# Kernel optimization log

Hardware: AMD Instinct MI355X
Metric: run time of the kernel (lower is better)

The kernel has to match this reference:

```python
import jax, jax.numpy as jnp
import numpy as np

B, T, D, H = 32, 512, 512, 1024


def setup_inputs() -> dict:
    key = jax.random.key(0)
    k1, k2, k3 = jax.random.split(key, 3)
    X = jax.random.normal(k1, (B, T, D), dtype=jnp.float32)
    # TF GRUCell variables: gates/kernel [D+H, 2H], gates/bias [2H] (init 1.0),
    # candidate/kernel [D+H, H], candidate/bias [H] (init 0.0). Use small random
    # values for a non-degenerate numerical baseline.
    gate_kernel = jax.random.normal(k2, (D + H, 2 * H), dtype=jnp.float32) * 0.02
    gate_bias = jnp.ones((2 * H,), dtype=jnp.float32)
    cand_kernel = jax.random.normal(k3, (D + H, H), dtype=jnp.float32) * 0.02
    cand_bias = jnp.zeros((H,), dtype=jnp.float32)
    return {"X": X, "gate_kernel": gate_kernel, "gate_bias": gate_bias,
            "cand_kernel": cand_kernel, "cand_bias": cand_bias}


def reference(X, gate_kernel, gate_bias, cand_kernel, cand_bias):
    """Static unidirectional GRU (TF GRUCell math), activation=tanh.
    Returns stacked per-step hidden states [B, T, H]; final state is out[:, -1]."""
    h0 = jnp.zeros((X.shape[0], cand_kernel.shape[1]), dtype=X.dtype)

    def step(h, x_t):
        # gates: r (reset), u (update) = sigmoid([x, h] @ Wg + bg)
        gates = jax.nn.sigmoid(jnp.concatenate([x_t, h], axis=-1) @ gate_kernel + gate_bias)
        r, u = jnp.split(gates, 2, axis=-1)
        # candidate: tanh([x, r*h] @ Wc + bc)
        c = jnp.tanh(jnp.concatenate([x_t, r * h], axis=-1) @ cand_kernel + cand_bias)
        h_new = u * h + (1.0 - u) * c
        return h_new, h_new

    _, hs = jax.lax.scan(step, h0, jnp.swapaxes(X, 0, 1))  # hs: [T, B, H]
    return jnp.swapaxes(hs, 0, 1)  # [B, T, H]
```

## Files before the change

### kernel.cpp

```cpp
#include <hip/hip_runtime.h>
#include <hip/hip_bf16.h>

typedef short s8v __attribute__((ext_vector_type(8)));
typedef float f4v __attribute__((ext_vector_type(4)));
typedef unsigned int u4v __attribute__((ext_vector_type(4)));
typedef unsigned int u2v __attribute__((ext_vector_type(2)));

#define NBLK 64
#define TPB 512

constexpr int BB = 32, TT = 512, DD = 512, HH = 1024;
constexpr int KK = DD + HH;
constexpr int PK = KK + 8;
constexpr int PK8 = PK / 8;
constexpr int K8 = KK / 8;

constexpr size_t OFF_WGT = 0;
constexpr size_t SZ_WGT  = (size_t)2 * HH * KK * 2;
constexpr size_t OFF_WCT = OFF_WGT + SZ_WGT;
constexpr size_t SZ_WCT  = (size_t)HH * KK * 2;
constexpr size_t OFF_XBF = OFF_WCT + SZ_WCT;
constexpr size_t SZ_XBF  = (size_t)BB * TT * DD * 2;
constexpr size_t OFF_HPB = OFF_XBF + SZ_XBF;
constexpr size_t SZ_PUB  = (size_t)BB * HH * 2;
constexpr size_t OFF_RPB = OFF_HPB + SZ_PUB;
constexpr size_t OFF_FLG = OFF_RPB + SZ_PUB;
constexpr size_t SZ_FLG  = (size_t)2 * NBLK * 2 * 16 * 4;

__global__ void wtr_kernel(const float* __restrict__ in, unsigned short* __restrict__ out, int N) {
    __shared__ float tl[32][33];
    int tx = threadIdx.x & 31, ty = threadIdx.x >> 5;
    int n0 = blockIdx.x * 32, k0 = blockIdx.y * 32;
#pragma unroll
    for (int r = ty; r < 32; r += 8) tl[r][tx] = in[(size_t)(k0 + r) * N + n0 + tx];
    __syncthreads();
#pragma unroll
    for (int r = ty; r < 32; r += 8) {
        __hip_bfloat16 h = __float2bfloat16(tl[tx][r]);
        out[(size_t)(n0 + r) * KK + k0 + tx] = *reinterpret_cast<unsigned short*>(&h);
    }
}

__global__ void xconv_kernel(const float* __restrict__ X, unsigned short* __restrict__ Xbf) {
    size_t i = ((size_t)blockIdx.x * 256 + threadIdx.x) * 4;
    float4 v = *reinterpret_cast<const float4*>(X + i);
    __hip_bfloat16 h0 = __float2bfloat16(v.x), h1 = __float2bfloat16(v.y);
    __hip_bfloat16 h2 = __float2bfloat16(v.z), h3 = __float2bfloat16(v.w);
    ushort4 o;
    o.x = *(unsigned short*)&h0; o.y = *(unsigned short*)&h1;
    o.z = *(unsigned short*)&h2; o.w = *(unsigned short*)&h3;
    *reinterpret_cast<ushort4*>(Xbf + i) = o;
}

__device__ __forceinline__ u4v cload16(const void* p) {
    u4v r; asm volatile("global_load_dwordx4 %0, %1, off sc0 sc1" : "=v"(r) : "v"(p) : "memory"); return r;
}
__device__ __forceinline__ void cstore8(void* p, u2v v) {
    asm volatile("global_store_dwordx2 %0, %1, off sc0 sc1" :: "v"(p), "v"(v) : "memory");
}
#define B16(x) __builtin_bit_cast(s8v, (x))
#define WAIT_VM(n) do { asm volatile("s_waitcnt vmcnt(" #n ")" ::: "memory"); \
                        __builtin_amdgcn_sched_barrier(0); } while (0)

__device__ __forceinline__ void poll16(const int* f, int blk0, int rtw, int gen, int lane) {
    if (lane < 16) {
        const int* fp = f + ((size_t)(blk0 + lane) * 2 + rtw) * 16;
        while (__hip_atomic_load(fp, __ATOMIC_RELAXED, __HIP_MEMORY_SCOPE_AGENT) < gen)
            __builtin_amdgcn_s_sleep(1);
    }
    asm volatile("" ::: "memory");
}

#define MFMA(A, B, C) __builtin_amdgcn_mfma_f32_16x16x32_bf16((A), (B), (C), 0, 0, 0)

__global__ __launch_bounds__(TPB, 1) void gru_kernel(
    const unsigned short* __restrict__ Xbf,
    const unsigned short* __restrict__ WgT,
    const unsigned short* __restrict__ WcT,
    const float* __restrict__ bg,
    const float* __restrict__ bc,
    float* __restrict__ out,
    unsigned short* __restrict__ hpub,
    unsigned short* __restrict__ rpub,
    int* __restrict__ gflagA,
    int* __restrict__ gflagB)
{
    __shared__ unsigned short sWg[32 * PK];
    __shared__ unsigned short sWc[16 * PK];
    __shared__ float sP[3][2][2][16][16];
    __shared__ unsigned short sStage[32][16];

    const int b    = blockIdx.x;
    const int tid  = threadIdx.x;
    const int wid  = tid >> 6;
    const int lane = tid & 63;
    const int l15  = lane & 15;
    const int lq   = lane >> 4;
    const int ks   = wid >> 1;
    const int rt   = wid & 1;
    const int roff = rt * 16;
    const int arow = roff + l15;
    const int bcol0= b * 16;

    {
        s8v* dst = (s8v*)sWg;
        for (int idx = tid; idx < 32 * K8; idx += TPB) {
            int c = idx / K8, k8 = idx % K8;
            int gc = (c < 16) ? (bcol0 + c) : (HH + bcol0 + (c - 16));
            dst[c * PK8 + k8] = ((const s8v*)(WgT + (size_t)gc * KK))[k8];
        }
        s8v* dst2 = (s8v*)sWc;
        for (int idx = tid; idx < 16 * K8; idx += TPB) {
            int c = idx / K8, k8 = idx % K8;
            dst2[c * PK8 + k8] = ((const s8v*)(WcT + (size_t)(bcol0 + c) * KK))[k8];
        }
    }

    const float bgr = bg[bcol0 + l15];
    const float bgu = bg[HH + bcol0 + l15];
    const float bcv = bc[bcol0 + l15];
    const int   ccol = bcol0 + l15;

    const s8v* sWg8 = (const s8v*)sWg;
    const s8v* sWc8 = (const s8v*)sWc;
    const s8v* bwr = sWg8 + l15 * PK8 + lq;
    const s8v* bwu = sWg8 + (16 + l15) * PK8 + lq;
    const s8v* bwc = sWc8 + l15 * PK8 + lq;
    const s8v* bwrx = bwr + 16 * ks;
    const s8v* bwux = bwu + 16 * ks;
    const s8v* bwrh = bwr + 64 + 32 * ks;
    const s8v* bwuh = bwu + 64 + 32 * ks;
    const s8v* bwcx = bwc + 16 * ks;
    const s8v* bwch = bwc + 64 + 32 * ks;

    float hprev[4] = {0.f, 0.f, 0.f, 0.f};
    float ureg[4]  = {0.f, 0.f, 0.f, 0.f};

    __syncthreads();

#pragma unroll 1
    for (int t = 0; t < TT; ++t) {
        const s8v* xk = (const s8v*)(Xbf + (size_t)arow * (TT * DD) + (size_t)t * DD) + lq + 16 * ks;

        f4v ar0 = {0,0,0,0}, ar1 = {0,0,0,0}, au0 = {0,0,0,0}, au1 = {0,0,0,0};
        {
            s8v x0 = xk[0], x1 = xk[4], x2 = xk[8], x3 = xk[12];
            ar0 = MFMA(x0, bwrx[0],  ar0); au0 = MFMA(x0, bwux[0],  au0);
            ar1 = MFMA(x1, bwrx[4],  ar1); au1 = MFMA(x1, bwux[4],  au1);
            ar0 = MFMA(x2, bwrx[8],  ar0); au0 = MFMA(x2, bwux[8],  au0);
            ar1 = MFMA(x3, bwrx[12], ar1); au1 = MFMA(x3, bwux[12], au1);
        }

        if (t > 0) {
            poll16(gflagB, ks * 16, rt, t, lane);
            const unsigned short* hp = hpub + (size_t)arow * HH + ks * 256 + lq * 8;
            u4v hb[8];
#pragma unroll
            for (int j = 0; j < 8; ++j) hb[j] = cload16(hp + (size_t)j * 32);
            WAIT_VM(4);
            ar0 = MFMA(B16(hb[0]), bwrh[0],  ar0); au0 = MFMA(B16(hb[0]), bwuh[0],  au0);
            ar1 = MFMA(B16(hb[1]), bwrh[4],  ar1); au1 = MFMA(B16(hb[1]), bwuh[4],  au1);
            ar0 = MFMA(B16(hb[2]), bwrh[8],  ar0); au0 = MFMA(B16(hb[2]), bwuh[8],  au0);
            ar1 = MFMA(B16(hb[3]), bwrh[12], ar1); au1 = MFMA(B16(hb[3]), bwuh[12], au1);
            WAIT_VM(0);
            ar0 = MFMA(B16(hb[4]), bwrh[16], ar0); au0 = MFMA(B16(hb[4]), bwuh[16], au0);
            ar1 = MFMA(B16(hb[5]), bwrh[20], ar1); au1 = MFMA(B16(hb[5]), bwuh[20], au1);
            ar0 = MFMA(B16(hb[6]), bwrh[24], ar0); au0 = MFMA(B16(hb[6]), bwuh[24], au0);
            ar1 = MFMA(B16(hb[7]), bwrh[28], ar1); au1 = MFMA(B16(hb[7]), bwuh[28], au1);
        }

        f4v pr = ar0 + ar1, pu = au0 + au1;
        if (ks > 0) {
#pragma unroll
            for (int i = 0; i < 4; ++i) {
                sP[ks - 1][rt][0][lq * 4 + i][l15] = pr[i];
                sP[ks - 1][rt][1][lq * 4 + i][l15] = pu[i];
            }
        }
        __syncthreads();
        float zr[4], zu[4];
        if (ks == 0) {
#pragma unroll
            for (int i = 0; i < 4; ++i) {
                int rr = lq * 4 + i;
                zr[i] = pr[i] + sP[0][rt][0][rr][l15] + sP[1][rt][0][rr][l15]
                              + sP[2][rt][0][rr][l15] + bgr;
                zu[i] = pu[i] + sP[0][rt][1][rr][l15] + sP[1][rt][1][rr][l15]
                              + sP[2][rt][1][rr][l15] + bgu;
            }
        }
        __syncthreads();
        if (ks == 0) {
#pragma unroll
            for (int i = 0; i < 4; ++i) {
                float r = 1.f / (1.f + __expf(-zr[i]));
                ureg[i] = 1.f / (1.f + __expf(-zu[i]));
                __hip_bfloat16 hb16 = __float2bfloat16(r * hprev[i]);
                sStage[roff + lq * 4 + i][l15] = *(unsigned short*)&hb16;
            }
            if (t > 0) {
                int prow = roff + (lane >> 2), pc4 = (lane & 3) * 4;
                u2v v = *reinterpret_cast<const u2v*>(&sStage[prow][pc4]);
                cstore8(rpub + (size_t)prow * HH + bcol0 + pc4, v);
                asm volatile("s_waitcnt vmcnt(0)" ::: "memory");
                if (lane == 0)
                    __hip_atomic_store(&gflagA[(b * 2 + rt) * 16], t,
                                       __ATOMIC_RELAXED, __HIP_MEMORY_SCOPE_AGENT);
            }
        }

        f4v c0 = {0,0,0,0}, c1 = {0,0,0,0};
        {
            s8v x0 = xk[0], x1 = xk[4], x2 = xk[8], x3 = xk[12];
            c0 = MFMA(x0, bwcx[0],  c0); c1 = MFMA(x1, bwcx[4],  c1);
            c0 = MFMA(x2, bwcx[8],  c0); c1 = MFMA(x3, bwcx[12], c1);
        }

        if (t > 0) {
            poll16(gflagA, ks * 16, rt, t, lane);
            const unsigned short* rp = rpub + (size_t)arow * HH + ks * 256 + lq * 8;
            u4v rb[8];
#pragma unroll
            for (int j = 0; j < 8; ++j) rb[j] = cload16(rp + (size_t)j * 32);
            WAIT_VM(4);
            c0 = MFMA(B16(rb[0]), bwch[0],  c0); c1 = MFMA(B16(rb[1]), bwch[4],  c1);
            c0 = MFMA(B16(rb[2]), bwch[8],  c0); c1 = MFMA(B16(rb[3]), bwch[12], c1);
            WAIT_VM(0);
            c0 = MFMA(B16(rb[4]), bwch[16], c0); c1 = MFMA(B16(rb[5]), bwch[20], c1);
            c0 = MFMA(B16(rb[6]), bwch[24], c0); c1 = MFMA(B16(rb[7]), bwch[28], c1);
        }

        f4v pc = c0 + c1;
        if (ks > 0) {
#pragma unroll
            for (int i = 0; i < 4; ++i) sP[ks - 1][rt][0][lq * 4 + i][l15] = pc[i];
        }
        __syncthreads();
        float zc[4];
        if (ks == 0) {
#pragma unroll
            for (int i = 0; i < 4; ++i) {
                int rr = lq * 4 + i;
                zc[i] = pc[i] + sP[0][rt][0][rr][l15] + sP[1][rt][0][rr][l15]
                              + sP[2][rt][0][rr][l15] + bcv;
            }
        }
        __syncthreads();
        if (ks == 0) {
#pragma unroll
            for (int i = 0; i < 4; ++i) {
                float e = __expf(2.f * zc[i]);
                float cv = 1.f - 2.f / (e + 1.f);
                float hn = ureg[i] * hprev[i] + (1.f - ureg[i]) * cv;
                hprev[i] = hn;
                __hip_bfloat16 hb16 = __float2bfloat16(hn);
                sStage[roff + lq * 4 + i][l15] = *(unsigned short*)&hb16;
            }
            int prow = roff + (lane >> 2), pc4 = (lane & 3) * 4;
            u2v v = *reinterpret_cast<const u2v*>(&sStage[prow][pc4]);
            cstore8(hpub + (size_t)prow * HH + bcol0 + pc4, v);
            asm volatile("s_waitcnt vmcnt(0)" ::: "memory");
            if (lane == 0)
                __hip_atomic_store(&gflagB[(b * 2 + rt) * 16], t + 1,
                                   __ATOMIC_RELAXED, __HIP_MEMORY_SCOPE_AGENT);
#pragma unroll
            for (int i = 0; i < 4; ++i) {
                int row = roff + lq * 4 + i;
                out[(size_t)row * (TT * HH) + (size_t)t * HH + ccol] = hprev[i];
            }
        }
    }
}

extern "C" void kernel_launch(void* const* d_in, const int* in_sizes, int n_in,
                              void* d_out, int out_size, void* d_ws, size_t ws_size,
                              hipStream_t stream) {
    const float* X  = (const float*)d_in[0];
    const float* gk = (const float*)d_in[1];
    const float* gb = (const float*)d_in[2];
    const float* ck = (const float*)d_in[3];
    const float* cb = (const float*)d_in[4];
    float* out = (float*)d_out;
    char* ws = (char*)d_ws;
    if (ws_size < OFF_FLG + SZ_FLG) return;

    unsigned short* WgT  = (unsigned short*)(ws + OFF_WGT);
    unsigned short* WcT  = (unsigned short*)(ws + OFF_WCT);
    unsigned short* Xbf  = (unsigned short*)(ws + OFF_XBF);
    unsigned short* hpub = (unsigned short*)(ws + OFF_HPB);
    unsigned short* rpub = (unsigned short*)(ws + OFF_RPB);
    int*            gflagA = (int*)(ws + OFF_FLG);
    int*            gflagB = gflagA + NBLK * 2 * 16;

    hipMemsetAsync(gflagA, 0, SZ_FLG, stream);

    dim3 tb(256);
    wtr_kernel<<<dim3(2 * HH / 32, KK / 32), tb, 0, stream>>>(gk, WgT, 2 * HH);
    wtr_kernel<<<dim3(HH / 32, KK / 32), tb, 0, stream>>>(ck, WcT, HH);
    xconv_kernel<<<(BB * TT * DD) / (256 * 4), tb, 0, stream>>>(X, Xbf);

    gru_kernel<<<NBLK, dim3(TPB), 0, stream>>>(Xbf, WgT, WcT, gb, cb, out,
                                               hpub, rpub, gflagA, gflagB);
}
```

Before: 3.914 ms.

## Exchange hidden state and reset gate between blocks as 8-bit quantized values

The per-step hidden state and reset gate that blocks publish to each other are now quantized to 8 bits instead of bf16. This halves the cross-block traffic on the latency-bound recurrence. Consumers decode the bytes to bf16 with integer-to-float tricks and fold the zero-point offset into a bias correction computed by a new weight-column-sum kernel. The global layout is also permuted so each lane loads contiguous 64-byte runs. This adds quantization error to the recurrent hidden state (about 1/127 resolution), which may push accuracy past tolerance, plus extra ALU work to decode.

Measured after the change: 4.188 ms. 1.07x slower.

```diff
diff --git a/kernel.cpp b/kernel.cpp
--- a/kernel.cpp
+++ b/kernel.cpp
@@ -4,7 +4,6 @@
 typedef short s8v __attribute__((ext_vector_type(8)));
 typedef float f4v __attribute__((ext_vector_type(4)));
 typedef unsigned int u4v __attribute__((ext_vector_type(4)));
-typedef unsigned int u2v __attribute__((ext_vector_type(2)));
 
 #define NBLK 64
 #define TPB 512
@@ -21,10 +20,12 @@
 constexpr size_t SZ_WCT  = (size_t)HH * KK * 2;
 constexpr size_t OFF_XBF = OFF_WCT + SZ_WCT;
 constexpr size_t SZ_XBF  = (size_t)BB * TT * DD * 2;
-constexpr size_t OFF_HPB = OFF_XBF + SZ_XBF;
-constexpr size_t SZ_PUB  = (size_t)BB * HH * 2;
-constexpr size_t OFF_RPB = OFF_HPB + SZ_PUB;
-constexpr size_t OFF_FLG = OFF_RPB + SZ_PUB;
+constexpr size_t OFF_SUM = OFF_XBF + SZ_XBF;
+constexpr size_t SZ_SUM  = (size_t)2 * HH * 4;
+constexpr size_t OFF_HP8 = OFF_SUM + SZ_SUM;
+constexpr size_t SZ_P8   = (size_t)BB * HH;
+constexpr size_t OFF_RP8 = OFF_HP8 + SZ_P8;
+constexpr size_t OFF_FLG = OFF_RP8 + SZ_P8;
 constexpr size_t SZ_FLG  = (size_t)2 * NBLK * 2 * 16 * 4;
 
 __global__ void wtr_kernel(const float* __restrict__ in, unsigned short* __restrict__ out, int N) {
@@ -52,10 +53,17 @@
     *reinterpret_cast<ushort4*>(Xbf + i) = o;
 }
 
+__global__ void sumw_kernel(const float* __restrict__ gk, float* __restrict__ sums) {
+    int col = blockIdx.x * 256 + threadIdx.x;
+    float s = 0.f;
+    for (int k = DD; k < KK; ++k) s += gk[(size_t)k * (2 * HH) + col];
+    sums[col] = s;
+}
+
 __device__ __forceinline__ u4v cload16(const void* p) {
     u4v r; asm volatile("global_load_dwordx4 %0, %1, off sc0 sc1" : "=v"(r) : "v"(p) : "memory"); return r;
 }
-__device__ __forceinline__ void cstore8(void* p, u2v v) {
+__device__ __forceinline__ void cstore8(void* p, unsigned long long v) {
     asm volatile("global_store_dwordx2 %0, %1, off sc0 sc1" :: "v"(p), "v"(v) : "memory");
 }
 #define B16(x) __builtin_bit_cast(s8v, (x))
@@ -73,22 +81,49 @@
 
 #define MFMA(A, B, C) __builtin_amdgcn_mfma_f32_16x16x32_bf16((A), (B), (C), 0, 0, 0)
 
+__device__ __forceinline__ unsigned int pkint(unsigned int w) {
+    float f0 = (float)(w & 0xffu);
+    float f1 = (float)((w >> 8) & 0xffu);
+    return __builtin_bit_cast(unsigned int, f1) | (__builtin_bit_cast(unsigned int, f0) >> 16);
+}
+__device__ __forceinline__ s8v hfrag(unsigned int d0, unsigned int d1) {
+    u4v u; u[0] = pkint(d0); u[1] = pkint(d0 >> 16); u[2] = pkint(d1); u[3] = pkint(d1 >> 16);
+    return __builtin_bit_cast(s8v, u);
+}
+__device__ __forceinline__ unsigned int pkrh(unsigned int hw, unsigned int rw) {
+    const float A  = 1.f / (127.f * 255.f);
+    const float Bc = -128.f / (127.f * 255.f);
+    float h0 = fmaf((float)(hw & 0xffu), A, Bc);
+    float h1 = fmaf((float)((hw >> 8) & 0xffu), A, Bc);
+    float p0 = h0 * (float)(rw & 0xffu);
+    float p1 = h1 * (float)((rw >> 8) & 0xffu);
+    return (__builtin_bit_cast(unsigned int, p1) & 0xffff0000u) |
+           (__builtin_bit_cast(unsigned int, p0) >> 16);
+}
+__device__ __forceinline__ s8v rhfrag(unsigned int hd0, unsigned int hd1,
+                                      unsigned int rd0, unsigned int rd1) {
+    u4v u; u[0] = pkrh(hd0, rd0); u[1] = pkrh(hd0 >> 16, rd0 >> 16);
+    u[2] = pkrh(hd1, rd1); u[3] = pkrh(hd1 >> 16, rd1 >> 16);
+    return __builtin_bit_cast(s8v, u);
+}
+
 __global__ __launch_bounds__(TPB, 1) void gru_kernel(
     const unsigned short* __restrict__ Xbf,
     const unsigned short* __restrict__ WgT,
     const unsigned short* __restrict__ WcT,
     const float* __restrict__ bg,
     const float* __restrict__ bc,
+    const float* __restrict__ sumw,
     float* __restrict__ out,
-    unsigned short* __restrict__ hpub,
-    unsigned short* __restrict__ rpub,
+    unsigned char* __restrict__ hp8,
+    unsigned char* __restrict__ rp8,
     int* __restrict__ gflagA,
     int* __restrict__ gflagB)
 {
     __shared__ unsigned short sWg[32 * PK];
     __shared__ unsigned short sWc[16 * PK];
     __shared__ float sP[3][2][2][16][16];
-    __shared__ unsigned short sStage[32][16];
+    __shared__ unsigned long long stgq[2][16][2];
 
     const int b    = blockIdx.x;
     const int tid  = threadIdx.x;
@@ -116,9 +151,11 @@
         }
     }
 
-    const float bgr = bg[bcol0 + l15];
-    const float bgu = bg[HH + bcol0 + l15];
-    const float bcv = bc[bcol0 + l15];
+    const float bgr  = bg[bcol0 + l15];
+    const float bgu  = bg[HH + bcol0 + l15];
+    const float bcv  = bc[bcol0 + l15];
+    const float corR = (128.f / 127.f) * sumw[bcol0 + l15];
+    const float corU = (128.f / 127.f) * sumw[HH + bcol0 + l15];
     const int   ccol = bcol0 + l15;
 
     const s8v* sWg8 = (const s8v*)sWg;
@@ -141,35 +178,40 @@
 #pragma unroll 1
     for (int t = 0; t < TT; ++t) {
         const s8v* xk = (const s8v*)(Xbf + (size_t)arow * (TT * DD) + (size_t)t * DD) + lq + 16 * ks;
-
-        f4v ar0 = {0,0,0,0}, ar1 = {0,0,0,0}, au0 = {0,0,0,0}, au1 = {0,0,0,0};
-        {
-            s8v x0 = xk[0], x1 = xk[4], x2 = xk[8], x3 = xk[12];
-            ar0 = MFMA(x0, bwrx[0],  ar0); au0 = MFMA(x0, bwux[0],  au0);
-            ar1 = MFMA(x1, bwrx[4],  ar1); au1 = MFMA(x1, bwux[4],  au1);
-            ar0 = MFMA(x2, bwrx[8],  ar0); au0 = MFMA(x2, bwux[8],  au0);
-            ar1 = MFMA(x3, bwrx[12], ar1); au1 = MFMA(x3, bwux[12], au1);
-        }
-
+        s8v x0 = xk[0], x1 = xk[4], x2 = xk[8], x3 = xk[12];
+
+        f4v axr = {0,0,0,0}, axu = {0,0,0,0}, ahr = {0,0,0,0}, ahu = {0,0,0,0};
+        u4v hq0, hq1, hq2, hq3;
         if (t > 0) {
             poll16(gflagB, ks * 16, rt, t, lane);
-            const unsigned short* hp = hpub + (size_t)arow * HH + ks * 256 + lq * 8;
-            u4v hb[8];
-#pragma unroll
-            for (int j = 0; j < 8; ++j) hb[j] = cload16(hp + (size_t)j * 32);
-            WAIT_VM(4);
-            ar0 = MFMA(B16(hb[0]), bwrh[0],  ar0); au0 = MFMA(B16(hb[0]), bwuh[0],  au0);
-            ar1 = MFMA(B16(hb[1]), bwrh[4],  ar1); au1 = MFMA(B16(hb[1]), bwuh[4],  au1);
-            ar0 = MFMA(B16(hb[2]), bwrh[8],  ar0); au0 = MFMA(B16(hb[2]), bwuh[8],  au0);
-            ar1 = MFMA(B16(hb[3]), bwrh[12], ar1); au1 = MFMA(B16(hb[3]), bwuh[12], au1);
+            const unsigned char* hp = hp8 + (size_t)arow * HH + lq * 256 + ks * 64;
+            hq0 = cload16(hp); hq1 = cload16(hp + 16);
+            hq2 = cload16(hp + 32); hq3 = cload16(hp + 48);
+            axr = MFMA(x0, bwrx[0],  axr); axu = MFMA(x0, bwux[0],  axu);
+            axr = MFMA(x1, bwrx[4],  axr); axu = MFMA(x1, bwux[4],  axu);
+            axr = MFMA(x2, bwrx[8],  axr); axu = MFMA(x2, bwux[8],  axu);
+            axr = MFMA(x3, bwrx[12], axr); axu = MFMA(x3, bwux[12], axu);
+            WAIT_VM(2);
+            { s8v f;
+              f = hfrag(hq0[0], hq0[1]); ahr = MFMA(f, bwrh[0],  ahr); ahu = MFMA(f, bwuh[0],  ahu);
+              f = hfrag(hq0[2], hq0[3]); ahr = MFMA(f, bwrh[4],  ahr); ahu = MFMA(f, bwuh[4],  ahu);
+              f = hfrag(hq1[0], hq1[1]); ahr = MFMA(f, bwrh[8],  ahr); ahu = MFMA(f, bwuh[8],  ahu);
+              f = hfrag(hq1[2], hq1[3]); ahr = MFMA(f, bwrh[12], ahr); ahu = MFMA(f, bwuh[12], ahu); }
             WAIT_VM(0);
-            ar0 = MFMA(B16(hb[4]), bwrh[16], ar0); au0 = MFMA(B16(hb[4]), bwuh[16], au0);
-            ar1 = MFMA(B16(hb[5]), bwrh[20], ar1); au1 = MFMA(B16(hb[5]), bwuh[20], au1);
-            ar0 = MFMA(B16(hb[6]), bwrh[24], ar0); au0 = MFMA(B16(hb[6]), bwuh[24], au0);
-            ar1 = MFMA(B16(hb[7]), bwrh[28], ar1); au1 = MFMA(B16(hb[7]), bwuh[28], au1);
-        }
-
-        f4v pr = ar0 + ar1, pu = au0 + au1;
+            { s8v f;
+              f = hfrag(hq2[0], hq2[1]); ahr = MFMA(f, bwrh[16], ahr); ahu = MFMA(f, bwuh[16], ahu);
+              f = hfrag(hq2[2], hq2[3]); ahr = MFMA(f, bwrh[20], ahr); ahu = MFMA(f, bwuh[20], ahu);
+              f = hfrag(hq3[0], hq3[1]); ahr = MFMA(f, bwrh[24], ahr); ahu = MFMA(f, bwuh[24], ahu);
+              f = hfrag(hq3[2], hq3[3]); ahr = MFMA(f, bwrh[28], ahr); ahu = MFMA(f, bwuh[28], ahu); }
+        } else {
+            axr = MFMA(x0, bwrx[0],  axr); axu = MFMA(x0, bwux[0],  axu);
+            axr = MFMA(x1, bwrx[4],  axr); axu = MFMA(x1, bwux[4],  axu);
+            axr = MFMA(x2, bwrx[8],  axr); axu = MFMA(x2, bwux[8],  axu);
+            axr = MFMA(x3, bwrx[12], axr); axu = MFMA(x3, bwux[12], axu);
+        }
+        f4v pr = axr + ahr * (1.f / 127.f);
+        f4v pu = axu + ahu * (1.f / 127.f);
+
         if (ks > 0) {
 #pragma unroll
             for (int i = 0; i < 4; ++i) {
@@ -180,13 +222,15 @@
         __syncthreads();
         float zr[4], zu[4];
         if (ks == 0) {
+            float br = (t > 0) ? (bgr - corR) : bgr;
+            float bu = (t > 0) ? (bgu - corU) : bgu;
 #pragma unroll
             for (int i = 0; i < 4; ++i) {
                 int rr = lq * 4 + i;
                 zr[i] = pr[i] + sP[0][rt][0][rr][l15] + sP[1][rt][0][rr][l15]
-                              + sP[2][rt][0][rr][l15] + bgr;
+                              + sP[2][rt][0][rr][l15] + br;
                 zu[i] = pu[i] + sP[0][rt][1][rr][l15] + sP[1][rt][1][rr][l15]
-                              + sP[2][rt][1][rr][l15] + bgu;
+                              + sP[2][rt][1][rr][l15] + bu;
             }
         }
         __syncthreads();
@@ -195,13 +239,15 @@
             for (int i = 0; i < 4; ++i) {
                 float r = 1.f / (1.f + __expf(-zr[i]));
                 ureg[i] = 1.f / (1.f + __expf(-zu[i]));
-                __hip_bfloat16 hb16 = __float2bfloat16(r * hprev[i]);
-                sStage[roff + lq * 4 + i][l15] = *(unsigned short*)&hb16;
+                float qr = __builtin_rintf(r * 255.f);
+                ((unsigned char*)&stgq[rt][lq * 4 + i][0])[l15] = (unsigned char)qr;
             }
             if (t > 0) {
-                int prow = roff + (lane >> 2), pc4 = (lane & 3) * 4;
-                u2v v = *reinterpret_cast<const u2v*>(&sStage[prow][pc4]);
-                cstore8(rpub + (size_t)prow * HH + bcol0 + pc4, v);
+                if (lane < 32) {
+                    int prow = lane >> 1, run = lane & 1;
+                    unsigned long long v = stgq[rt][prow][run];
+                    cstore8(rp8 + (size_t)(roff + prow) * HH + ((b & 1) * 2 + run) * 256 + (b >> 1) * 8, v);
+                }
                 asm volatile("s_waitcnt vmcnt(0)" ::: "memory");
                 if (lane == 0)
                     __hip_atomic_store(&gflagA[(b * 2 + rt) * 16], t,
@@ -209,28 +255,32 @@
             }
         }
 
-        f4v c0 = {0,0,0,0}, c1 = {0,0,0,0};
-        {
-            s8v x0 = xk[0], x1 = xk[4], x2 = xk[8], x3 = xk[12];
-            c0 = MFMA(x0, bwcx[0],  c0); c1 = MFMA(x1, bwcx[4],  c1);
-            c0 = MFMA(x2, bwcx[8],  c0); c1 = MFMA(x3, bwcx[12], c1);
-        }
-
+        f4v cx = {0,0,0,0}, ch = {0,0,0,0};
         if (t > 0) {
             poll16(gflagA, ks * 16, rt, t, lane);
-            const unsigned short* rp = rpub + (size_t)arow * HH + ks * 256 + lq * 8;
-            u4v rb[8];
-#pragma unroll
-            for (int j = 0; j < 8; ++j) rb[j] = cload16(rp + (size_t)j * 32);
-            WAIT_VM(4);
-            c0 = MFMA(B16(rb[0]), bwch[0],  c0); c1 = MFMA(B16(rb[1]), bwch[4],  c1);
-            c0 = MFMA(B16(rb[2]), bwch[8],  c0); c1 = MFMA(B16(rb[3]), bwch[12], c1);
+            const unsigned char* rp = rp8 + (size_t)arow * HH + lq * 256 + ks * 64;
+            u4v rq0 = cload16(rp),      rq1 = cload16(rp + 16);
+            u4v rq2 = cload16(rp + 32), rq3 = cload16(rp + 48);
+            cx = MFMA(x0, bwcx[0],  cx); cx = MFMA(x1, bwcx[4],  cx);
+            cx = MFMA(x2, bwcx[8],  cx); cx = MFMA(x3, bwcx[12], cx);
+            WAIT_VM(2);
+            { s8v f;
+              f = rhfrag(hq0[0], hq0[1], rq0[0], rq0[1]); ch = MFMA(f, bwch[0],  ch);
+              f = rhfrag(hq0[2], hq0[3], rq0[2], rq0[3]); ch = MFMA(f, bwch[4],  ch);
+              f = rhfrag(hq1[0], hq1[1], rq1[0], rq1[1]); ch = MFMA(f, bwch[8],  ch);
+              f = rhfrag(hq1[2], hq1[3], rq1[2], rq1[3]); ch = MFMA(f, bwch[12], ch); }
             WAIT_VM(0);
-            c0 = MFMA(B16(rb[4]), bwch[16], c0); c1 = MFMA(B16(rb[5]), bwch[20], c1);
-            c0 = MFMA(B16(rb[6]), bwch[24], c0); c1 = MFMA(B16(rb[7]), bwch[28], c1);
-        }
-
-        f4v pc = c0 + c1;
+            { s8v f;
+              f = rhfrag(hq2[0], hq2[1], rq2[0], rq2[1]); ch = MFMA(f, bwch[16], ch);
+              f = rhfrag(hq2[2], hq2[3], rq2[2], rq2[3]); ch = MFMA(f, bwch[20], ch);
+              f = rhfrag(hq3[0], hq3[1], rq3[0], rq3[1]); ch = MFMA(f, bwch[24], ch);
+              f = rhfrag(hq3[2], hq3[3], rq3[2], rq3[3]); ch = MFMA(f, bwch[28], ch); }
+        } else {
+            cx = MFMA(x0, bwcx[0],  cx); cx = MFMA(x1, bwcx[4],  cx);
+            cx = MFMA(x2, bwcx[8],  cx); cx = MFMA(x3, bwcx[12], cx);
+        }
+        f4v pc = cx + ch;
+
         if (ks > 0) {
 #pragma unroll
             for (int i = 0; i < 4; ++i) sP[ks - 1][rt][0][lq * 4 + i][l15] = pc[i];
@@ -253,12 +303,14 @@
                 float cv = 1.f - 2.f / (e + 1.f);
                 float hn = ureg[i] * hprev[i] + (1.f - ureg[i]) * cv;
                 hprev[i] = hn;
-                __hip_bfloat16 hb16 = __float2bfloat16(hn);
-                sStage[roff + lq * 4 + i][l15] = *(unsigned short*)&hb16;
-            }
-            int prow = roff + (lane >> 2), pc4 = (lane & 3) * 4;
-            u2v v = *reinterpret_cast<const u2v*>(&sStage[prow][pc4]);
-            cstore8(hpub + (size_t)prow * HH + bcol0 + pc4, v);
+                float qh = __builtin_rintf(hn * 127.f) + 128.f;
+                ((unsigned char*)&stgq[rt][lq * 4 + i][0])[l15] = (unsigned char)qh;
+            }
+            if (lane < 32) {
+                int prow = lane >> 1, run = lane & 1;
+                unsigned long long v = stgq[rt][prow][run];
+                cstore8(hp8 + (size_t)(roff + prow) * HH + ((b & 1) * 2 + run) * 256 + (b >> 1) * 8, v);
+            }
             asm volatile("s_waitcnt vmcnt(0)" ::: "memory");
             if (lane == 0)
                 __hip_atomic_store(&gflagB[(b * 2 + rt) * 16], t + 1,
@@ -287,8 +339,9 @@
     unsigned short* WgT  = (unsigned short*)(ws + OFF_WGT);
     unsigned short* WcT  = (unsigned short*)(ws + OFF_WCT);
     unsigned short* Xbf  = (unsigned short*)(ws + OFF_XBF);
-    unsigned short* hpub = (unsigned short*)(ws + OFF_HPB);
-    unsigned short* rpub = (unsigned short*)(ws + OFF_RPB);
+    float*          sums = (float*)(ws + OFF_SUM);
+    unsigned char*  hp8  = (unsigned char*)(ws + OFF_HP8);
+    unsigned char*  rp8  = (unsigned char*)(ws + OFF_RP8);
     int*            gflagA = (int*)(ws + OFF_FLG);
     int*            gflagB = gflagA + NBLK * 2 * 16;
 
@@ -298,7 +351,8 @@
     wtr_kernel<<<dim3(2 * HH / 32, KK / 32), tb, 0, stream>>>(gk, WgT, 2 * HH);
     wtr_kernel<<<dim3(HH / 32, KK / 32), tb, 0, stream>>>(ck, WcT, HH);
     xconv_kernel<<<(BB * TT * DD) / (256 * 4), tb, 0, stream>>>(X, Xbf);
-
-    gru_kernel<<<NBLK, dim3(TPB), 0, stream>>>(Xbf, WgT, WcT, gb, cb, out,
-                                               hpub, rpub, gflagA, gflagB);
-}
+    sumw_kernel<<<dim3(2 * HH / 256), tb, 0, stream>>>(gk, sums);
+
+    gru_kernel<<<NBLK, dim3(TPB), 0, stream>>>(Xbf, WgT, WcT, gb, cb, sums, out,
+                                               hp8, rp8, gflagA, gflagB);
+}
```

## Use per-timestep publish buffers so h/r loads can use cached plain loads

Applied to the files above, without the earlier changes.

Adds a DEEP variant that gives every timestep its own slot in the h and r publish buffers. Because each address is written only once, consumers can use ordinary cached vector loads instead of coherent sc0/sc1 loads. It also issues the h/r loads right after polling and overlaps them with the x-projection MFMAs before waiting. This costs 64 MB of workspace per buffer, and it relies on fresh addresses never being stale in non-coherent caches; the path is only taken when the workspace is large enough.

Result: slower. 4.025 ms (+2.8%).

```diff
diff --git a/kernel.cpp b/kernel.cpp
--- a/kernel.cpp
+++ b/kernel.cpp
@@ -14,6 +14,7 @@
 constexpr int PK = KK + 8;
 constexpr int PK8 = PK / 8;
 constexpr int K8 = KK / 8;
+constexpr size_t BBHH = (size_t)BB * HH;
 
 constexpr size_t OFF_WGT = 0;
 constexpr size_t SZ_WGT  = (size_t)2 * HH * KK * 2;
@@ -22,10 +23,15 @@
 constexpr size_t OFF_XBF = OFF_WCT + SZ_WCT;
 constexpr size_t SZ_XBF  = (size_t)BB * TT * DD * 2;
 constexpr size_t OFF_HPB = OFF_XBF + SZ_XBF;
-constexpr size_t SZ_PUB  = (size_t)BB * HH * 2;
-constexpr size_t OFF_RPB = OFF_HPB + SZ_PUB;
-constexpr size_t OFF_FLG = OFF_RPB + SZ_PUB;
+constexpr size_t SZ_PUB1 = BBHH * 2;
+constexpr size_t SZ_PUBT = SZ_PUB1 * TT;
 constexpr size_t SZ_FLG  = (size_t)2 * NBLK * 2 * 16 * 4;
+constexpr size_t OFF_RPB_D = OFF_HPB + SZ_PUBT;
+constexpr size_t OFF_FLG_D = OFF_RPB_D + SZ_PUBT;
+constexpr size_t NEED_D    = OFF_FLG_D + SZ_FLG;
+constexpr size_t OFF_RPB_S = OFF_HPB + SZ_PUB1;
+constexpr size_t OFF_FLG_S = OFF_RPB_S + SZ_PUB1;
+constexpr size_t NEED_S    = OFF_FLG_S + SZ_FLG;
 
 __global__ void wtr_kernel(const float* __restrict__ in, unsigned short* __restrict__ out, int N) {
     __shared__ float tl[32][33];
@@ -73,6 +79,7 @@
 
 #define MFMA(A, B, C) __builtin_amdgcn_mfma_f32_16x16x32_bf16((A), (B), (C), 0, 0, 0)
 
+template<bool DEEP>
 __global__ __launch_bounds__(TPB, 1) void gru_kernel(
     const unsigned short* __restrict__ Xbf,
     const unsigned short* __restrict__ WgT,
@@ -88,7 +95,7 @@
     __shared__ unsigned short sWg[32 * PK];
     __shared__ unsigned short sWc[16 * PK];
     __shared__ float sP[3][2][2][16][16];
-    __shared__ unsigned short sStage[32][16];
+    __shared__ unsigned short sStage[2][16][16];
 
     const int b    = blockIdx.x;
     const int tid  = threadIdx.x;
@@ -116,9 +123,9 @@
         }
     }
 
-    const float bgr = bg[bcol0 + l15];
-    const float bgu = bg[HH + bcol0 + l15];
-    const float bcv = bc[bcol0 + l15];
+    const float bgr  = bg[bcol0 + l15];
+    const float bgu  = bg[HH + bcol0 + l15];
+    const float bcv  = bc[bcol0 + l15];
     const int   ccol = bcol0 + l15;
 
     const s8v* sWg8 = (const s8v*)sWg;
@@ -141,32 +148,43 @@
 #pragma unroll 1
     for (int t = 0; t < TT; ++t) {
         const s8v* xk = (const s8v*)(Xbf + (size_t)arow * (TT * DD) + (size_t)t * DD) + lq + 16 * ks;
+        s8v x0 = xk[0], x1 = xk[4], x2 = xk[8], x3 = xk[12];
 
         f4v ar0 = {0,0,0,0}, ar1 = {0,0,0,0}, au0 = {0,0,0,0}, au1 = {0,0,0,0};
-        {
-            s8v x0 = xk[0], x1 = xk[4], x2 = xk[8], x3 = xk[12];
+        if (t > 0) {
+            poll16(gflagB, ks * 16, rt, t, lane);
+            const unsigned short* hp = hpub + (DEEP ? (size_t)(t - 1) * BBHH : 0)
+                                     + (size_t)arow * HH + ks * 256 + lq * 8;
+            u4v hb[8];
+            if (DEEP) {
+#pragma unroll
+                for (int j = 0; j < 8; ++j) hb[j] = *reinterpret_cast<const u4v*>(hp + (size_t)j * 32);
+                ar0 = MFMA(x0, bwrx[0],  ar0); au0 = MFMA(x0, bwux[0],  au0);
+                ar1 = MFMA(x1, bwrx[4],  ar1); au1 = MFMA(x1, bwux[4],  au1);
+                ar0 = MFMA(x2, bwrx[8],  ar0); au0 = MFMA(x2, bwux[8],  au0);
+                ar1 = MFMA(x3, bwrx[12], ar1); au1 = MFMA(x3, bwux[12], au1);
+            } else {
+#pragma unroll
+                for (int j = 0; j < 8; ++j) hb[j] = cload16(hp + (size_t)j * 32);
+                ar0 = MFMA(x0, bwrx[0],  ar0); au0 = MFMA(x0, bwux[0],  au0);
+                ar1 = MFMA(x1, bwrx[4],  ar1); au1 = MFMA(x1, bwux[4],  au1);
+                ar0 = MFMA(x2, bwrx[8],  ar0); au0 = MFMA(x2, bwux[8],  au0);
+                ar1 = MFMA(x3, bwrx[12], ar1); au1 = MFMA(x3, bwux[12], au1);
+                WAIT_VM(0);
+            }
+            ar0 = MFMA(B16(hb[0]), bwrh[0],  ar0); au0 = MFMA(B16(hb[0]), bwuh[0],  au0);
+            ar1 = MFMA(B16(hb[1]), bwrh[4],  ar1); au1 = MFMA(B16(hb[1]), bwuh[4],  au1);
+            ar0 = MFMA(B16(hb[2]), bwrh[8],  ar0); au0 = MFMA(B16(hb[2]), bwuh[8],  au0);
+            ar1 = MFMA(B16(hb[3]), bwrh[12], ar1); au1 = MFMA(B16(hb[3]), bwuh[12], au1);
+            ar0 = MFMA(B16(hb[4]), bwrh[16], ar0); au0 = MFMA(B16(hb[4]), bwuh[16], au0);
+            ar1 = MFMA(B16(hb[5]), bwrh[20], ar1); au1 = MFMA(B16(hb[5]), bwuh[20], au1);
+            ar0 = MFMA(B16(hb[6]), bwrh[24], ar0); au0 = MFMA(B16(hb[6]), bwuh[24], au0);
+            ar1 = MFMA(B16(hb[7]), bwrh[28], ar1); au1 = MFMA(B16(hb[7]), bwuh[28], au1);
+        } else {
             ar0 = MFMA(x0, bwrx[0],  ar0); au0 = MFMA(x0, bwux[0],  au0);
             ar1 = MFMA(x1, bwrx[4],  ar1); au1 = MFMA(x1, bwux[4],  au1);
             ar0 = MFMA(x2, bwrx[8],  ar0); au0 = MFMA(x2, bwux[8],  au0);
             ar1 = MFMA(x3, bwrx[12], ar1); au1 = MFMA(x3, bwux[12], au1);
-        }
-
-        if (t > 0) {
-            poll16(gflagB, ks * 16, rt, t, lane);
-            const unsigned short* hp = hpub + (size_t)arow * HH + ks * 256 + lq * 8;
-            u4v hb[8];
-#pragma unroll
-            for (int j = 0; j < 8; ++j) hb[j] = cload16(hp + (size_t)j * 32);
-            WAIT_VM(4);
-            ar0 = MFMA(B16(hb[0]), bwrh[0],  ar0); au0 = MFMA(B16(hb[0]), bwuh[0],  au0);
-            ar1 = MFMA(B16(hb[1]), bwrh[4],  ar1); au1 = MFMA(B16(hb[1]), bwuh[4],  au1);
-            ar0 = MFMA(B16(hb[2]), bwrh[8],  ar0); au0 = MFMA(B16(hb[2]), bwuh[8],  au0);
-            ar1 = MFMA(B16(hb[3]), bwrh[12], ar1); au1 = MFMA(B16(hb[3]), bwuh[12], au1);
-            WAIT_VM(0);
-            ar0 = MFMA(B16(hb[4]), bwrh[16], ar0); au0 = MFMA(B16(hb[4]), bwuh[16], au0);
-            ar1 = MFMA(B16(hb[5]), bwrh[20], ar1); au1 = MFMA(B16(hb[5]), bwuh[20], au1);
-            ar0 = MFMA(B16(hb[6]), bwrh[24], ar0); au0 = MFMA(B16(hb[6]), bwuh[24], au0);
-            ar1 = MFMA(B16(hb[7]), bwrh[28], ar1); au1 = MFMA(B16(hb[7]), bwuh[28], au1);
         }
 
         f4v pr = ar0 + ar1, pu = au0 + au1;
@@ -196,12 +214,13 @@
                 float r = 1.f / (1.f + __expf(-zr[i]));
                 ureg[i] = 1.f / (1.f + __expf(-zu[i]));
                 __hip_bfloat16 hb16 = __float2bfloat16(r * hprev[i]);
-                sStage[roff + lq * 4 + i][l15] = *(unsigned short*)&hb16;
+                sStage[rt][lq * 4 + i][l15] = *(unsigned short*)&hb16;
             }
             if (t > 0) {
-                int prow = roff + (lane >> 2), pc4 = (lane & 3) * 4;
-                u2v v = *reinterpret_cast<const u2v*>(&sStage[prow][pc4]);
-                cstore8(rpub + (size_t)prow * HH + bcol0 + pc4, v);
+                int prow = lane >> 2, pc4 = (lane & 3) * 4;
+                u2v v = *reinterpret_cast<const u2v*>(&sStage[rt][prow][pc4]);
+                cstore8(rpub + (DEEP ? (size_t)t * BBHH : 0)
+                             + (size_t)(roff + prow) * HH + bcol0 + pc4, v);
                 asm volatile("s_waitcnt vmcnt(0)" ::: "memory");
                 if (lane == 0)
                     __hip_atomic_store(&gflagA[(b * 2 + rt) * 16], t,
@@ -210,24 +229,30 @@
         }
 
         f4v c0 = {0,0,0,0}, c1 = {0,0,0,0};
-        {
-            s8v x0 = xk[0], x1 = xk[4], x2 = xk[8], x3 = xk[12];
+        if (t > 0) {
+            poll16(gflagA, ks * 16, rt, t, lane);
+            const unsigned short* rp = rpub + (DEEP ? (size_t)t * BBHH : 0)
+                                     + (size_t)arow * HH + ks * 256 + lq * 8;
+            u4v rb[8];
+            if (DEEP) {
+#pragma unroll
+                for (int j = 0; j < 8; ++j) rb[j] = *reinterpret_cast<const u4v*>(rp + (size_t)j * 32);
+                c0 = MFMA(x0, bwcx[0],  c0); c1 = MFMA(x1, bwcx[4],  c1);
+                c0 = MFMA(x2, bwcx[8],  c0); c1 = MFMA(x3, bwcx[12], c1);
+            } else {
+#pragma unroll
+                for (int j = 0; j < 8; ++j) rb[j] = cload16(rp + (size_t)j * 32);
+                c0 = MFMA(x0, bwcx[0],  c0); c1 = MFMA(x1, bwcx[4],  c1);
+                c0 = MFMA(x2, bwcx[8],  c0); c1 = MFMA(x3, bwcx[12], c1);
+                WAIT_VM(0);
+            }
+            c0 = MFMA(B16(rb[0]), bwch[0],  c0); c1 = MFMA(B16(rb[1]), bwch[4],  c1);
+            c0 = MFMA(B16(rb[2]), bwch[8],  c0); c1 = MFMA(B16(rb[3]), bwch[12], c1);
+            c0 = MFMA(B16(rb[4]), bwch[16], c0); c1 = MFMA(B16(rb[5]), bwch[20], c1);
+            c0 = MFMA(B16(rb[6]), bwch[24], c0); c1 = MFMA(B16(rb[7]), bwch[28], c1);
+        } else {
             c0 = MFMA(x0, bwcx[0],  c0); c1 = MFMA(x1, bwcx[4],  c1);
             c0 = MFMA(x2, bwcx[8],  c0); c1 = MFMA(x3, bwcx[12], c1);
-        }
-
-        if (t > 0) {
-            poll16(gflagA, ks * 16, rt, t, lane);
-            const unsigned short* rp = rpub + (size_t)arow * HH + ks * 256 + lq * 8;
-            u4v rb[8];
-#pragma unroll
-            for (int j = 0; j < 8; ++j) rb[j] = cload16(rp + (size_t)j * 32);
-            WAIT_VM(4);
-            c0 = MFMA(B16(rb[0]), bwch[0],  c0); c1 = MFMA(B16(rb[1]), bwch[4],  c1);
-            c0 = MFMA(B16(rb[2]), bwch[8],  c0); c1 = MFMA(B16(rb[3]), bwch[12], c1);
-            WAIT_VM(0);
-            c0 = MFMA(B16(rb[4]), bwch[16], c0); c1 = MFMA(B16(rb[5]), bwch[20], c1);
-            c0 = MFMA(B16(rb[6]), bwch[24], c0); c1 = MFMA(B16(rb[7]), bwch[28], c1);
         }
 
         f4v pc = c0 + c1;
@@ -254,11 +279,12 @@
                 float hn = ureg[i] * hprev[i] + (1.f - ureg[i]) * cv;
                 hprev[i] = hn;
                 __hip_bfloat16 hb16 = __float2bfloat16(hn);
-                sStage[roff + lq * 4 + i][l15] = *(unsigned short*)&hb16;
-            }
-            int prow = roff + (lane >> 2), pc4 = (lane & 3) * 4;
-            u2v v = *reinterpret_cast<const u2v*>(&sStage[prow][pc4]);
-            cstore8(hpub + (size_t)prow * HH + bcol0 + pc4, v);
+                sStage[rt][lq * 4 + i][l15] = *(unsigned short*)&hb16;
+            }
+            int prow = lane >> 2, pc4 = (lane & 3) * 4;
+            u2v v = *reinterpret_cast<const u2v*>(&sStage[rt][prow][pc4]);
+            cstore8(hpub + (DEEP ? (size_t)t * BBHH : 0)
+                         + (size_t)(roff + prow) * HH + bcol0 + pc4, v);
             asm volatile("s_waitcnt vmcnt(0)" ::: "memory");
             if (lane == 0)
                 __hip_atomic_store(&gflagB[(b * 2 + rt) * 16], t + 1,
@@ -282,14 +308,16 @@
     const float* cb = (const float*)d_in[4];
     float* out = (float*)d_out;
     char* ws = (char*)d_ws;
-    if (ws_size < OFF_FLG + SZ_FLG) return;
+    if (ws_size < NEED_S) return;
+
+    const bool deep = (ws_size >= NEED_D);
 
     unsigned short* WgT  = (unsigned short*)(ws + OFF_WGT);
     unsigned short* WcT  = (unsigned short*)(ws + OFF_WCT);
     unsigned short* Xbf  = (unsigned short*)(ws + OFF_XBF);
     unsigned short* hpub = (unsigned short*)(ws + OFF_HPB);
-    unsigned short* rpub = (unsigned short*)(ws + OFF_RPB);
-    int*            gflagA = (int*)(ws + OFF_FLG);
+    unsigned short* rpub = (unsigned short*)(ws + (deep ? OFF_RPB_D : OFF_RPB_S));
+    int*            gflagA = (int*)(ws + (deep ? OFF_FLG_D : OFF_FLG_S));
     int*            gflagB = gflagA + NBLK * 2 * 16;
 
     hipMemsetAsync(gflagA, 0, SZ_FLG, stream);
@@ -299,6 +327,10 @@
     wtr_kernel<<<dim3(HH / 32, KK / 32), tb, 0, stream>>>(ck, WcT, HH);
     xconv_kernel<<<(BB * TT * DD) / (256 * 4), tb, 0, stream>>>(X, Xbf);
 
-    gru_kernel<<<NBLK, dim3(TPB), 0, stream>>>(Xbf, WgT, WcT, gb, cb, out,
-                                               hpub, rpub, gflagA, gflagB);
-}
+    if (deep)
+        gru_kernel<true><<<NBLK, dim3(TPB), 0, stream>>>(Xbf, WgT, WcT, gb, cb, out,
+                                                         hpub, rpub, gflagA, gflagB);
+    else
+        gru_kernel<false><<<NBLK, dim3(TPB), 0, stream>>>(Xbf, WgT, WcT, gb, cb, out,
+                                                          hpub, rpub, gflagA, gflagB);
+}
```

## Distribute gate epilogue across all warps and split r/u phases with per-warp flags

Applied to the files above, without the earlier changes.

The final reduction and activation work, previously done only by the ks==0 warps, is now spread across all eight warps so each warp finishes a quarter of the rows and publishes its own slice of r*h and h with its own flag. Flags are packed four per row-tile so consumers poll one dwordx4 load instead of a padded single flag. The reset gate is computed and published before the update-gate MFMAs, so the r-publish leaves the critical path sooner, and the update partials are stored in bf16 in shared memory. In exchange there are more flag stores per step, an extra barrier at the end of each step, and reduced precision for the update-gate partial sums.

Result: slower. 4.113 ms (+5.1%).

```diff
diff --git a/kernel.cpp b/kernel.cpp
--- a/kernel.cpp
+++ b/kernel.cpp
@@ -25,7 +25,7 @@
 constexpr size_t SZ_PUB  = (size_t)BB * HH * 2;
 constexpr size_t OFF_RPB = OFF_HPB + SZ_PUB;
 constexpr size_t OFF_FLG = OFF_RPB + SZ_PUB;
-constexpr size_t SZ_FLG  = (size_t)2 * NBLK * 2 * 16 * 4;
+constexpr size_t SZ_FLG  = (size_t)2 * NBLK * 8 * 4;
 
 __global__ void wtr_kernel(const float* __restrict__ in, unsigned short* __restrict__ out, int N) {
     __shared__ float tl[32][33];
@@ -58,20 +58,32 @@
 __device__ __forceinline__ void cstore8(void* p, u2v v) {
     asm volatile("global_store_dwordx2 %0, %1, off sc0 sc1" :: "v"(p), "v"(v) : "memory");
 }
+__device__ __forceinline__ void cstore4(void* p, int v) {
+    asm volatile("global_store_dword %0, %1, off sc0 sc1" :: "v"(p), "v"(v) : "memory");
+}
 #define B16(x) __builtin_bit_cast(s8v, (x))
 #define WAIT_VM(n) do { asm volatile("s_waitcnt vmcnt(" #n ")" ::: "memory"); \
                         __builtin_amdgcn_sched_barrier(0); } while (0)
 
-__device__ __forceinline__ void poll16(const int* f, int blk0, int rtw, int gen, int lane) {
+__device__ __forceinline__ void pollq(const int* flags, int blk0, int rtw, int gen, int lane) {
     if (lane < 16) {
-        const int* fp = f + ((size_t)(blk0 + lane) * 2 + rtw) * 16;
-        while (__hip_atomic_load(fp, __ATOMIC_RELAXED, __HIP_MEMORY_SCOPE_AGENT) < gen)
+        const int* fp = flags + (size_t)(blk0 + lane) * 8 + rtw * 4;
+        while (true) {
+            u4v f; asm volatile("global_load_dwordx4 %0, %1, off sc0 sc1\ns_waitcnt vmcnt(0)"
+                                : "=v"(f) : "v"(fp) : "memory");
+            if ((int)f[0] >= gen && (int)f[1] >= gen && (int)f[2] >= gen && (int)f[3] >= gen) break;
             __builtin_amdgcn_s_sleep(1);
+        }
     }
     asm volatile("" ::: "memory");
 }
 
 #define MFMA(A, B, C) __builtin_amdgcn_mfma_f32_16x16x32_bf16((A), (B), (C), 0, 0, 0)
+
+__device__ __forceinline__ float bfu2f(unsigned short u) {
+    unsigned int w = (unsigned int)u << 16;
+    return __builtin_bit_cast(float, w);
+}
 
 __global__ __launch_bounds__(TPB, 1) void gru_kernel(
     const unsigned short* __restrict__ Xbf,
@@ -87,8 +99,9 @@
 {
     __shared__ unsigned short sWg[32 * PK];
     __shared__ unsigned short sWc[16 * PK];
-    __shared__ float sP[3][2][2][16][16];
-    __shared__ unsigned short sStage[32][16];
+    __shared__ float sPrc[4][2][16][16];
+    __shared__ unsigned short sPu[4][2][16][16];
+    __shared__ unsigned short stage[8][4][16];
 
     const int b    = blockIdx.x;
     const int tid  = threadIdx.x;
@@ -98,9 +111,11 @@
     const int lq   = lane >> 4;
     const int ks   = wid >> 1;
     const int rt   = wid & 1;
-    const int roff = rt * 16;
-    const int arow = roff + l15;
+    const int arow = rt * 16 + l15;
     const int bcol0= b * 16;
+    const int finm = ks * 4 + (lane >> 4);
+    const int finrow = rt * 16 + finm;
+    const int fincol = bcol0 + l15;
 
     {
         s8v* dst = (s8v*)sWg;
@@ -116,10 +131,9 @@
         }
     }
 
-    const float bgr = bg[bcol0 + l15];
-    const float bgu = bg[HH + bcol0 + l15];
-    const float bcv = bc[bcol0 + l15];
-    const int   ccol = bcol0 + l15;
+    const float bgr = bg[fincol];
+    const float bgu = bg[HH + fincol];
+    const float bcv = bc[fincol];
 
     const s8v* sWg8 = (const s8v*)sWg;
     const s8v* sWc8 = (const s8v*)sWc;
@@ -133,91 +147,81 @@
     const s8v* bwcx = bwc + 16 * ks;
     const s8v* bwch = bwc + 64 + 32 * ks;
 
-    float hprev[4] = {0.f, 0.f, 0.f, 0.f};
-    float ureg[4]  = {0.f, 0.f, 0.f, 0.f};
+    float hprev = 0.f;
 
     __syncthreads();
 
 #pragma unroll 1
     for (int t = 0; t < TT; ++t) {
         const s8v* xk = (const s8v*)(Xbf + (size_t)arow * (TT * DD) + (size_t)t * DD) + lq + 16 * ks;
-
-        f4v ar0 = {0,0,0,0}, ar1 = {0,0,0,0}, au0 = {0,0,0,0}, au1 = {0,0,0,0};
-        {
-            s8v x0 = xk[0], x1 = xk[4], x2 = xk[8], x3 = xk[12];
-            ar0 = MFMA(x0, bwrx[0],  ar0); au0 = MFMA(x0, bwux[0],  au0);
-            ar1 = MFMA(x1, bwrx[4],  ar1); au1 = MFMA(x1, bwux[4],  au1);
-            ar0 = MFMA(x2, bwrx[8],  ar0); au0 = MFMA(x2, bwux[8],  au0);
-            ar1 = MFMA(x3, bwrx[12], ar1); au1 = MFMA(x3, bwux[12], au1);
-        }
-
+        s8v x0 = xk[0], x1 = xk[4], x2 = xk[8], x3 = xk[12];
+
+        f4v ar0 = {0,0,0,0}, ar1 = {0,0,0,0};
+        ar0 = MFMA(x0, bwrx[0],  ar0); ar1 = MFMA(x1, bwrx[4],  ar1);
+        ar0 = MFMA(x2, bwrx[8],  ar0); ar1 = MFMA(x3, bwrx[12], ar1);
+        u4v hb[8];
         if (t > 0) {
-            poll16(gflagB, ks * 16, rt, t, lane);
+            pollq(gflagB, ks * 16, rt, t, lane);
             const unsigned short* hp = hpub + (size_t)arow * HH + ks * 256 + lq * 8;
-            u4v hb[8];
 #pragma unroll
             for (int j = 0; j < 8; ++j) hb[j] = cload16(hp + (size_t)j * 32);
             WAIT_VM(4);
-            ar0 = MFMA(B16(hb[0]), bwrh[0],  ar0); au0 = MFMA(B16(hb[0]), bwuh[0],  au0);
-            ar1 = MFMA(B16(hb[1]), bwrh[4],  ar1); au1 = MFMA(B16(hb[1]), bwuh[4],  au1);
-            ar0 = MFMA(B16(hb[2]), bwrh[8],  ar0); au0 = MFMA(B16(hb[2]), bwuh[8],  au0);
-            ar1 = MFMA(B16(hb[3]), bwrh[12], ar1); au1 = MFMA(B16(hb[3]), bwuh[12], au1);
+            ar0 = MFMA(B16(hb[0]), bwrh[0],  ar0); ar1 = MFMA(B16(hb[1]), bwrh[4],  ar1);
+            ar0 = MFMA(B16(hb[2]), bwrh[8],  ar0); ar1 = MFMA(B16(hb[3]), bwrh[12], ar1);
             WAIT_VM(0);
-            ar0 = MFMA(B16(hb[4]), bwrh[16], ar0); au0 = MFMA(B16(hb[4]), bwuh[16], au0);
-            ar1 = MFMA(B16(hb[5]), bwrh[20], ar1); au1 = MFMA(B16(hb[5]), bwuh[20], au1);
-            ar0 = MFMA(B16(hb[6]), bwrh[24], ar0); au0 = MFMA(B16(hb[6]), bwuh[24], au0);
-            ar1 = MFMA(B16(hb[7]), bwrh[28], ar1); au1 = MFMA(B16(hb[7]), bwuh[28], au1);
-        }
-
-        f4v pr = ar0 + ar1, pu = au0 + au1;
-        if (ks > 0) {
-#pragma unroll
-            for (int i = 0; i < 4; ++i) {
-                sP[ks - 1][rt][0][lq * 4 + i][l15] = pr[i];
-                sP[ks - 1][rt][1][lq * 4 + i][l15] = pu[i];
+            ar0 = MFMA(B16(hb[4]), bwrh[16], ar0); ar1 = MFMA(B16(hb[5]), bwrh[20], ar1);
+            ar0 = MFMA(B16(hb[6]), bwrh[24], ar0); ar1 = MFMA(B16(hb[7]), bwrh[28], ar1);
+        }
+        f4v pr = ar0 + ar1;
+#pragma unroll
+        for (int i = 0; i < 4; ++i) sPrc[ks][rt][lq * 4 + i][l15] = pr[i];
+        __syncthreads();
+
+        {
+            float zr = sPrc[0][rt][finm][l15] + sPrc[1][rt][finm][l15]
+                     + sPrc[2][rt][finm][l15] + sPrc[3][rt][finm][l15] + bgr;
+            float r = 1.f / (1.f + __expf(-zr));
+            __hip_bfloat16 hb16 = __float2bfloat16(r * hprev);
+            stage[wid][lane >> 4][l15] = *(unsigned short*)&hb16;
+            if (t > 0) {
+                if (lane < 16) {
+                    u2v v = *reinterpret_cast<const u2v*>(&stage[wid][lane >> 2][(lane & 3) * 4]);
+                    cstore8(rpub + (size_t)(rt * 16 + ks * 4 + (lane >> 2)) * HH + bcol0 + (lane & 3) * 4, v);
+                }
+                asm volatile("s_waitcnt vmcnt(0)" ::: "memory");
+                if (lane == 0) cstore4(gflagA + b * 8 + rt * 4 + ks, t);
             }
         }
-        __syncthreads();
-        float zr[4], zu[4];
-        if (ks == 0) {
-#pragma unroll
-            for (int i = 0; i < 4; ++i) {
-                int rr = lq * 4 + i;
-                zr[i] = pr[i] + sP[0][rt][0][rr][l15] + sP[1][rt][0][rr][l15]
-                              + sP[2][rt][0][rr][l15] + bgr;
-                zu[i] = pu[i] + sP[0][rt][1][rr][l15] + sP[1][rt][1][rr][l15]
-                              + sP[2][rt][1][rr][l15] + bgu;
-            }
-        }
-        __syncthreads();
-        if (ks == 0) {
-#pragma unroll
-            for (int i = 0; i < 4; ++i) {
-                float r = 1.f / (1.f + __expf(-zr[i]));
-                ureg[i] = 1.f / (1.f + __expf(-zu[i]));
-                __hip_bfloat16 hb16 = __float2bfloat16(r * hprev[i]);
-                sStage[roff + lq * 4 + i][l15] = *(unsigned short*)&hb16;
-            }
-            if (t > 0) {
-                int prow = roff + (lane >> 2), pc4 = (lane & 3) * 4;
-                u2v v = *reinterpret_cast<const u2v*>(&sStage[prow][pc4]);
-                cstore8(rpub + (size_t)prow * HH + bcol0 + pc4, v);
-                asm volatile("s_waitcnt vmcnt(0)" ::: "memory");
-                if (lane == 0)
-                    __hip_atomic_store(&gflagA[(b * 2 + rt) * 16], t,
-                                       __ATOMIC_RELAXED, __HIP_MEMORY_SCOPE_AGENT);
-            }
-        }
-
+
+        f4v au0 = {0,0,0,0}, au1 = {0,0,0,0};
+        au0 = MFMA(x0, bwux[0],  au0); au1 = MFMA(x1, bwux[4],  au1);
+        au0 = MFMA(x2, bwux[8],  au0); au1 = MFMA(x3, bwux[12], au1);
+        if (t > 0) {
+            au0 = MFMA(B16(hb[0]), bwuh[0],  au0); au1 = MFMA(B16(hb[1]), bwuh[4],  au1);
+            au0 = MFMA(B16(hb[2]), bwuh[8],  au0); au1 = MFMA(B16(hb[3]), bwuh[12], au1);
+            au0 = MFMA(B16(hb[4]), bwuh[16], au0); au1 = MFMA(B16(hb[5]), bwuh[20], au1);
+            au0 = MFMA(B16(hb[6]), bwuh[24], au0); au1 = MFMA(B16(hb[7]), bwuh[28], au1);
+        }
+        f4v pu = au0 + au1;
+#pragma unroll
+        for (int i = 0; i < 4; ++i) {
+            __hip_bfloat16 ub = __float2bfloat16(pu[i]);
+            sPu[ks][rt][lq * 4 + i][l15] = *(unsigned short*)&ub;
+        }
         f4v c0 = {0,0,0,0}, c1 = {0,0,0,0};
+        c0 = MFMA(x0, bwcx[0],  c0); c1 = MFMA(x1, bwcx[4],  c1);
+        c0 = MFMA(x2, bwcx[8],  c0); c1 = MFMA(x3, bwcx[12], c1);
+        __syncthreads();
+
+        float ureg;
         {
-            s8v x0 = xk[0], x1 = xk[4], x2 = xk[8], x3 = xk[12];
-            c0 = MFMA(x0, bwcx[0],  c0); c1 = MFMA(x1, bwcx[4],  c1);
-            c0 = MFMA(x2, bwcx[8],  c0); c1 = MFMA(x3, bwcx[12], c1);
+            float zu = bfu2f(sPu[0][rt][finm][l15]) + bfu2f(sPu[1][rt][finm][l15])
+                     + bfu2f(sPu[2][rt][finm][l15]) + bfu2f(sPu[3][rt][finm][l15]) + bgu;
+            ureg = 1.f / (1.f + __expf(-zu));
         }
 
         if (t > 0) {
-            poll16(gflagA, ks * 16, rt, t, lane);
+            pollq(gflagA, ks * 16, rt, t, lane);
             const unsigned short* rp = rpub + (size_t)arow * HH + ks * 256 + lq * 8;
             u4v rb[8];
 #pragma unroll
@@ -229,46 +233,29 @@
             c0 = MFMA(B16(rb[4]), bwch[16], c0); c1 = MFMA(B16(rb[5]), bwch[20], c1);
             c0 = MFMA(B16(rb[6]), bwch[24], c0); c1 = MFMA(B16(rb[7]), bwch[28], c1);
         }
-
         f4v pc = c0 + c1;
-        if (ks > 0) {
-#pragma unroll
-            for (int i = 0; i < 4; ++i) sP[ks - 1][rt][0][lq * 4 + i][l15] = pc[i];
-        }
-        __syncthreads();
-        float zc[4];
-        if (ks == 0) {
-#pragma unroll
-            for (int i = 0; i < 4; ++i) {
-                int rr = lq * 4 + i;
-                zc[i] = pc[i] + sP[0][rt][0][rr][l15] + sP[1][rt][0][rr][l15]
-                              + sP[2][rt][0][rr][l15] + bcv;
+#pragma unroll
+        for (int i = 0; i < 4; ++i) sPrc[ks][rt][lq * 4 + i][l15] = pc[i];
+        __syncthreads();
+
+        {
+            float zc = sPrc[0][rt][finm][l15] + sPrc[1][rt][finm][l15]
+                     + sPrc[2][rt][finm][l15] + sPrc[3][rt][finm][l15] + bcv;
+            float e = __expf(2.f * zc);
+            float cv = 1.f - 2.f / (e + 1.f);
+            float hn = ureg * hprev + (1.f - ureg) * cv;
+            hprev = hn;
+            __hip_bfloat16 hb16 = __float2bfloat16(hn);
+            stage[wid][lane >> 4][l15] = *(unsigned short*)&hb16;
+            if (lane < 16) {
+                u2v v = *reinterpret_cast<const u2v*>(&stage[wid][lane >> 2][(lane & 3) * 4]);
+                cstore8(hpub + (size_t)(rt * 16 + ks * 4 + (lane >> 2)) * HH + bcol0 + (lane & 3) * 4, v);
             }
-        }
-        __syncthreads();
-        if (ks == 0) {
-#pragma unroll
-            for (int i = 0; i < 4; ++i) {
-                float e = __expf(2.f * zc[i]);
-                float cv = 1.f - 2.f / (e + 1.f);
-                float hn = ureg[i] * hprev[i] + (1.f - ureg[i]) * cv;
-                hprev[i] = hn;
-                __hip_bfloat16 hb16 = __float2bfloat16(hn);
-                sStage[roff + lq * 4 + i][l15] = *(unsigned short*)&hb16;
-            }
-            int prow = roff + (lane >> 2), pc4 = (lane & 3) * 4;
-            u2v v = *reinterpret_cast<const u2v*>(&sStage[prow][pc4]);
-            cstore8(hpub + (size_t)prow * HH + bcol0 + pc4, v);
             asm volatile("s_waitcnt vmcnt(0)" ::: "memory");
-            if (lane == 0)
-                __hip_atomic_store(&gflagB[(b * 2 + rt) * 16], t + 1,
-                                   __ATOMIC_RELAXED, __HIP_MEMORY_SCOPE_AGENT);
-#pragma unroll
-            for (int i = 0; i < 4; ++i) {
-                int row = roff + lq * 4 + i;
-                out[(size_t)row * (TT * HH) + (size_t)t * HH + ccol] = hprev[i];
-            }
-        }
+            if (lane == 0) cstore4(gflagB + b * 8 + rt * 4 + ks, t + 1);
+            out[(size_t)finrow * (TT * HH) + (size_t)t * HH + fincol] = hn;
+        }
+        __syncthreads();
     }
 }
 
@@ -290,7 +277,7 @@
     unsigned short* hpub = (unsigned short*)(ws + OFF_HPB);
     unsigned short* rpub = (unsigned short*)(ws + OFF_RPB);
     int*            gflagA = (int*)(ws + OFF_FLG);
-    int*            gflagB = gflagA + NBLK * 2 * 16;
+    int*            gflagB = gflagA + NBLK * 8;
 
     hipMemsetAsync(gflagA, 0, SZ_FLG, stream);
 
```
